# Performance work log

Measured on AMD Instinct MI355X. Metric: run time of the kernel, lower is better.

Reference implementation:

```python
import jax, jax.numpy as jnp
import numpy as np

B = 1024          # number of graphs
H = 8             # heads
EPS = 1e-5        # LayerNorm eps (torch default)
MEAN_RES_SCALE = 0.2


def _ln(x, w, b):
    mu = x.mean(-1, keepdims=True)
    var = ((x - mu) ** 2).mean(-1, keepdims=True)
    return (x - mu) / jnp.sqrt(var + EPS) * w + b


def setup_inputs() -> dict:
    key = jax.random.key(0)
    ks = jax.random.split(key, 10)
    N, D = 262144, 256
    s = 1.0 / np.sqrt(D)
    return {
        "h": jax.random.normal(ks[0], (N, D), jnp.float32),
        "batch": jnp.sort(jax.random.randint(ks[1], (N,), 0, B)),
        "cdr_mask": jax.random.bernoulli(ks[2], 0.2, (N,)),
        "iface_mask": jax.random.bernoulli(ks[3], 0.2, (N,)),
        "ln_kv_w": jnp.ones((D,), jnp.float32),
        "ln_kv_b": jnp.zeros((D,), jnp.float32),
        "ln_q_w": jnp.ones((D,), jnp.float32),
        "ln_q_b": jnp.zeros((D,), jnp.float32),
        "Wk": jax.random.normal(ks[4], (D, D), jnp.float32) * s,
        "Wv": jax.random.normal(ks[5], (D, D), jnp.float32) * s,
        "Wq": jax.random.normal(ks[6], (D, 2 * D), jnp.float32) * (1.0 / np.sqrt(2 * D)),
        "Wres": jax.random.normal(ks[7], (D, D), jnp.float32) * s,
        "Wout": jax.random.normal(ks[8], (D, D), jnp.float32) * s,
        "cdr_bias": jnp.asarray(0.6, jnp.float32),
        "iface_bias": jnp.asarray(0.8, jnp.float32),
        "logit_scale": jnp.asarray(1.0, jnp.float32),
    }


def reference(h, batch, cdr_mask, iface_mask, ln_kv_w, ln_kv_b, ln_q_w, ln_q_b,
              Wk, Wv, Wq, Wres, Wout, cdr_bias, iface_bias, logit_scale):
    N, D = h.shape
    hd = D // H
    # per-graph mean / max pooling (segment reductions; all segments non-empty)
    counts = jax.ops.segment_sum(jnp.ones((N,), h.dtype), batch, num_segments=B)[:, None]
    mean_raw = jax.ops.segment_sum(h, batch, num_segments=B) / counts      # [B,D]
    max_raw = jax.ops.segment_max(h, batch, num_segments=B)                # [B,D]
    # single query per graph (dropout = identity in eval)
    q = jnp.concatenate([mean_raw, max_raw], axis=-1) @ Wq.T               # [B,D]
    q = _ln(q, ln_q_w, ln_q_b).reshape(B, H, hd)                           # [B,H,hd]
    # keys / values per node
    h_ln = _ln(h, ln_kv_w, ln_kv_b)
    k = (h_ln @ Wk.T).reshape(N, H, hd)
    v = (h_ln @ Wv.T).reshape(N, H, hd)
    # attention logits with mask biases
    logit = (k * q[batch]).sum(-1) * (logit_scale / np.sqrt(hd))           # [N,H]
    logit = logit + cdr_bias * cdr_mask.astype(h.dtype)[:, None]
    logit = logit + iface_bias * iface_mask.astype(h.dtype)[:, None]
    # segment softmax over nodes of each graph
    m = jax.ops.segment_max(logit, batch, num_segments=B)                  # [B,H]
    e = jnp.exp(logit - m[batch])
    z = jax.ops.segment_sum(e, batch, num_segments=B)                      # [B,H]
    attn = e / z[batch]                                                    # [N,H]
    g = jax.ops.segment_sum(attn[..., None] * v, batch, num_segments=B)    # [B,H,hd]
    g = g.reshape(B, D)
    return g @ Wout.T + MEAN_RES_SCALE * (mean_raw @ Wres.T)               # [B,D]
```

## Files before the change

### kernel.cpp

```cpp
#include <hip/hip_runtime.h>
#include <math.h>

#define D 256
#define BGRAPH 1024
#define H 8
#define NW 4
#define CDIM 2304

static constexpr float EPS = 1e-5f;
static constexpr float MEAN_RES_SCALE = 0.2f;
static constexpr float INV_SQRT_HD = 0.17677669529663687f;
static constexpr float DEFER_THR = 8.0f;

__global__ void k_offsets(const int* __restrict__ batch, int* __restrict__ offs, int N) {
    int n = blockIdx.x * blockDim.x + threadIdx.x;
    if (n >= N) return;
    int bn = batch[n];
    if (bn < 0) bn = 0;
    if (bn >= BGRAPH) bn = BGRAPH - 1;
    if (n == 0) {
        offs[BGRAPH] = N;
        for (int bb = 0; bb <= bn; ++bb) offs[bb] = 0;
    } else {
        int bp = batch[n - 1];
        if (bp < 0) bp = 0;
        if (bp >= BGRAPH) bp = BGRAPH - 1;
        if (bp != bn)
            for (int bb = bp + 1; bb <= bn; ++bb) offs[bb] = n;
    }
    if (n == N - 1)
        for (int bb = bn + 1; bb < BGRAPH; ++bb) offs[bb] = N;
}

__global__ __launch_bounds__(256) void k_pool(
    const float4* __restrict__ h4, const int* __restrict__ offs,
    const float* __restrict__ Wq, const float* __restrict__ lnq_w,
    const float* __restrict__ lnq_b, const float* __restrict__ Wk,
    const float* __restrict__ logit_scale,
    float* __restrict__ Wkq_g, float* __restrict__ App) {
    __shared__ alignas(16) float psum[NW][D];
    __shared__ alignas(16) float pmax[NW][D];
    __shared__ alignas(16) float cat_s[2 * D];
    __shared__ alignas(16) float q_s[D];
    __shared__ float red_s[2 * NW];

    int b = blockIdx.x;
    int t = threadIdx.x;
    int l = t & 63, w = t >> 6;
    int s = offs[b], e = offs[b + 1];
    int cnt = e - s;

    float4 sum4 = {0.f, 0.f, 0.f, 0.f};
    float4 max4 = {-INFINITY, -INFINITY, -INFINITY, -INFINITY};
    int n = s + w;
    for (; n + NW < e; n += 2 * NW) {
        float4 x0 = h4[(size_t)n * 64 + l];
        float4 x1 = h4[(size_t)(n + NW) * 64 + l];
        sum4.x += x0.x + x1.x; sum4.y += x0.y + x1.y;
        sum4.z += x0.z + x1.z; sum4.w += x0.w + x1.w;
        max4.x = fmaxf(max4.x, fmaxf(x0.x, x1.x));
        max4.y = fmaxf(max4.y, fmaxf(x0.y, x1.y));
        max4.z = fmaxf(max4.z, fmaxf(x0.z, x1.z));
        max4.w = fmaxf(max4.w, fmaxf(x0.w, x1.w));
    }
    if (n < e) {
        float4 x0 = h4[(size_t)n * 64 + l];
        sum4.x += x0.x; sum4.y += x0.y; sum4.z += x0.z; sum4.w += x0.w;
        max4.x = fmaxf(max4.x, x0.x); max4.y = fmaxf(max4.y, x0.y);
        max4.z = fmaxf(max4.z, x0.z); max4.w = fmaxf(max4.w, x0.w);
    }
    *(float4*)&psum[w][4 * l] = sum4;
    *(float4*)&pmax[w][4 * l] = max4;
    __syncthreads();

    int d = t;
    float ssum = psum[0][d] + psum[1][d] + psum[2][d] + psum[3][d];
    float smax = fmaxf(fmaxf(pmax[0][d], pmax[1][d]), fmaxf(pmax[2][d], pmax[3][d]));
    float mean = ssum / (cnt > 0 ? (float)cnt : 1.f);
    if (cnt == 0) { mean = 0.f; smax = 0.f; }
    cat_s[d] = mean;
    cat_s[D + d] = smax;
    App[(size_t)b * CDIM + 2048 + d] = MEAN_RES_SCALE * mean;
    __syncthreads();

    float qp = 0.f;
    const float4* wq4 = (const float4*)(Wq + (size_t)d * 2 * D);
    #pragma unroll 4
    for (int jj = 0; jj < 128; ++jj) {
        float4 wv = wq4[jj];
        float4 cv = *(const float4*)&cat_s[4 * jj];
        qp += wv.x * cv.x + wv.y * cv.y + wv.z * cv.z + wv.w * cv.w;
    }
    float v1 = qp, v2 = qp * qp;
    #pragma unroll
    for (int dd = 1; dd < 64; dd <<= 1) {
        v1 += __shfl_xor(v1, dd);
        v2 += __shfl_xor(v2, dd);
    }
    if (l == 0) { red_s[w] = v1; red_s[NW + w] = v2; }
    __syncthreads();
    float S1 = red_s[0] + red_s[1] + red_s[2] + red_s[3];
    float S2 = red_s[4] + red_s[5] + red_s[6] + red_s[7];
    float mu = S1 * (1.f / D);
    float var = S2 * (1.f / D) - mu * mu;
    float rstd = rsqrtf(var + EPS);
    q_s[d] = (qp - mu) * rstd * lnq_w[d] + lnq_b[d];
    __syncthreads();

    float scale = logit_scale[0] * INV_SQRT_HD;
    int j = t;
    #pragma unroll
    for (int hh = 0; hh < H; ++hh) {
        float acc = 0.f;
        #pragma unroll 8
        for (int r = 0; r < 32; ++r)
            acc += q_s[hh * 32 + r] * Wk[(size_t)(hh * 32 + r) * D + j];
        Wkq_g[(size_t)b * 2048 + hh * D + j] = acc * scale;
    }
}

__device__ __forceinline__ float reduce8(float v[8], int l) {
    {
        bool hi = (l & 1) != 0;
        #pragma unroll
        for (int c = 0; c < 4; ++c) {
            float send = hi ? v[2 * c] : v[2 * c + 1];
            float keep = hi ? v[2 * c + 1] : v[2 * c];
            v[c] = keep + __shfl_xor(send, 1);
        }
    }
    {
        bool hi = (l & 2) != 0;
        #pragma unroll
        for (int c = 0; c < 2; ++c) {
            float send = hi ? v[2 * c] : v[2 * c + 1];
            float keep = hi ? v[2 * c + 1] : v[2 * c];
            v[c] = keep + __shfl_xor(send, 2);
        }
    }
    {
        bool hi = (l & 4) != 0;
        float send = hi ? v[0] : v[1];
        float keep = hi ? v[1] : v[0];
        v[0] = keep + __shfl_xor(send, 4);
    }
    v[0] += __shfl_xor(v[0], 8);
    v[0] += __shfl_xor(v[0], 16);
    v[0] += __shfl_xor(v[0], 32);
    return v[0];
}

__device__ __forceinline__ float reduce2(float a, float b, int l) {
    bool hi = (l & 1) != 0;
    float send = hi ? a : b;
    float keep = hi ? b : a;
    float r = keep + __shfl_xor(send, 1);
    r += __shfl_xor(r, 2);
    r += __shfl_xor(r, 4);
    r += __shfl_xor(r, 8);
    r += __shfl_xor(r, 16);
    r += __shfl_xor(r, 32);
    return r;
}

__global__ __launch_bounds__(256, 4) void k_attn(
    const float4* __restrict__ h4, const int* __restrict__ offs,
    const float* __restrict__ lnkv_w, const float* __restrict__ lnkv_b,
    const int* __restrict__ cdr_mask, const int* __restrict__ iface_mask,
    const float* __restrict__ cdr_bias, const float* __restrict__ iface_bias,
    const float* __restrict__ Wkq_g, float* __restrict__ App) {
    __shared__ union alignas(16) {
        float wkq[H * D];
        float amrg[NW - 1][H * D];
    } u;
    __shared__ alignas(16) float evb[NW][8];
    __shared__ alignas(16) float scb[NW][8];
    __shared__ float mz_s[NW][H];
    __shared__ float zz_s[NW][H];

    int b = blockIdx.x;
    int t = threadIdx.x;
    int l = t & 63, w = t >> 6;
    for (int i = t; i < H * D; i += 256) u.wkq[i] = Wkq_g[(size_t)b * 2048 + i];
    int s = offs[b], e = offs[b + 1];
    float cb = cdr_bias[0], ib = iface_bias[0];
    float4 w4 = *(const float4*)&lnkv_w[4 * l];
    float4 b4 = *(const float4*)&lnkv_b[4 * l];
    __syncthreads();

    if (s == e) {
        for (int i = t; i < H * D; i += 256) App[(size_t)b * CDIM + i] = 0.f;
        return;
    }

    float4 wwkq[H];
    float c1p[H], c0p[H];
    #pragma unroll
    for (int hh = 0; hh < H; ++hh) {
        float4 kq = *(const float4*)&u.wkq[hh * D + 4 * l];
        wwkq[hh].x = w4.x * kq.x; wwkq[hh].y = w4.y * kq.y;
        wwkq[hh].z = w4.z * kq.z; wwkq[hh].w = w4.w * kq.w;
        c1p[hh] = wwkq[hh].x + wwkq[hh].y + wwkq[hh].z + wwkq[hh].w;
        c0p[hh] = b4.x * kq.x + b4.y * kq.y + b4.z * kq.z + b4.w * kq.w;
    }
    float myc1 = reduce8(c1p, l);
    float myc0 = reduce8(c0p, l);

    float mref = -INFINITY, z = 0.f;
    float4 A4[H];
    #pragma unroll
    for (int hh = 0; hh < H; ++hh) A4[hh] = {0.f, 0.f, 0.f, 0.f};

    int n = s + w;
    float4 x = {0.f, 0.f, 0.f, 0.f};
    float bias = 0.f;
    if (n < e) {
        x = h4[(size_t)n * 64 + l];
        bias = cb * (float)cdr_mask[n] + ib * (float)iface_mask[n];
    }
    for (; n < e; n += NW) {
        int n2 = n + NW;
        float4 xn = {0.f, 0.f, 0.f, 0.f};
        float biasn = 0.f;
        if (n2 < e) {
            xn = h4[(size_t)n2 * 64 + l];
            biasn = cb * (float)cdr_mask[n2] + ib * (float)iface_mask[n2];
        }

        float v[8];
        #pragma unroll
        for (int hh = 0; hh < H; ++hh)
            v[hh] = x.x * wwkq[hh].x + x.y * wwkq[hh].y +
                    x.z * wwkq[hh].z + x.w * wwkq[hh].w;
        float s1p = x.x + x.y + x.z + x.w;
        float s2p = x.x * x.x + x.y * x.y + x.z * x.z + x.w * x.w;
        float r = reduce8(v, l);
        float rs = reduce2(s1p, s2p, l);
        float s1 = __shfl(rs, l & ~1);
        float s2 = __shfl(rs, l | 1);
        float mu = s1 * (1.f / D);
        float var = s2 * (1.f / D) - mu * mu;
        float a = rsqrtf(var + EPS);
        float lg = fmaf(r - mu * myc1, a, myc0) + bias;

        unsigned long long need = __ballot(lg > mref + DEFER_THR);
        if (need) {
            float nm = fmaxf(mref, lg);
            float sc = __expf(mref - nm);
            if (l < 8) scb[w][l] = sc;
            mref = nm;
            z *= sc;
            float4 sa = *(float4*)&scb[w][0];
            float4 sb = *(float4*)&scb[w][4];
            A4[0].x *= sa.x; A4[0].y *= sa.x; A4[0].z *= sa.x; A4[0].w *= sa.x;
            A4[1].x *= sa.y; A4[1].y *= sa.y; A4[1].z *= sa.y; A4[1].w *= sa.y;
            A4[2].x *= sa.z; A4[2].y *= sa.z; A4[2].z *= sa.z; A4[2].w *= sa.z;
            A4[3].x *= sa.w; A4[3].y *= sa.w; A4[3].z *= sa.w; A4[3].w *= sa.w;
            A4[4].x *= sb.x; A4[4].y *= sb.x; A4[4].z *= sb.x; A4[4].w *= sb.x;
            A4[5].x *= sb.y; A4[5].y *= sb.y; A4[5].z *= sb.y; A4[5].w *= sb.y;
            A4[6].x *= sb.z; A4[6].y *= sb.z; A4[6].z *= sb.z; A4[6].w *= sb.z;
            A4[7].x *= sb.w; A4[7].y *= sb.w; A4[7].z *= sb.w; A4[7].w *= sb.w;
        }
        float ev = __expf(lg - mref);
        if (l < 8) evb[w][l] = ev;
        z += ev;
        float4 ea = *(float4*)&evb[w][0];
        float4 eb = *(float4*)&evb[w][4];
        float cc = -mu * a;
        float4 hl;
        hl.x = fmaf(fmaf(x.x, a, cc), w4.x, b4.x);
        hl.y = fmaf(fmaf(x.y, a, cc), w4.y, b4.y);
        hl.z = fmaf(fmaf(x.z, a, cc), w4.z, b4.z);
        hl.w = fmaf(fmaf(x.w, a, cc), w4.w, b4.w);
        A4[0].x = fmaf(ea.x, hl.x, A4[0].x); A4[0].y = fmaf(ea.x, hl.y, A4[0].y);
        A4[0].z = fmaf(ea.x, hl.z, A4[0].z); A4[0].w = fmaf(ea.x, hl.w, A4[0].w);
        A4[1].x = fmaf(ea.y, hl.x, A4[1].x); A4[1].y = fmaf(ea.y, hl.y, A4[1].y);
        A4[1].z = fmaf(ea.y, hl.z, A4[1].z); A4[1].w = fmaf(ea.y, hl.w, A4[1].w);
        A4[2].x = fmaf(ea.z, hl.x, A4[2].x); A4[2].y = fmaf(ea.z, hl.y, A4[2].y);
        A4[2].z = fmaf(ea.z, hl.z, A4[2].z); A4[2].w = fmaf(ea.z, hl.w, A4[2].w);
        A4[3].x = fmaf(ea.w, hl.x, A4[3].x); A4[3].y = fmaf(ea.w, hl.y, A4[3].y);
        A4[3].z = fmaf(ea.w, hl.z, A4[3].z); A4[3].w = fmaf(ea.w, hl.w, A4[3].w);
        A4[4].x = fmaf(eb.x, hl.x, A4[4].x); A4[4].y = fmaf(eb.x, hl.y, A4[4].y);
        A4[4].z = fmaf(eb.x, hl.z, A4[4].z); A4[4].w = fmaf(eb.x, hl.w, A4[4].w);
        A4[5].x = fmaf(eb.y, hl.x, A4[5].x); A4[5].y = fmaf(eb.y, hl.y, A4[5].y);
        A4[5].z = fmaf(eb.y, hl.z, A4[5].z); A4[5].w = fmaf(eb.y, hl.w, A4[5].w);
        A4[6].x = fmaf(eb.z, hl.x, A4[6].x); A4[6].y = fmaf(eb.z, hl.y, A4[6].y);
        A4[6].z = fmaf(eb.z, hl.z, A4[6].z); A4[6].w = fmaf(eb.z, hl.w, A4[6].w);
        A4[7].x = fmaf(eb.w, hl.x, A4[7].x); A4[7].y = fmaf(eb.w, hl.y, A4[7].y);
        A4[7].z = fmaf(eb.w, hl.z, A4[7].z); A4[7].w = fmaf(eb.w, hl.w, A4[7].w);

        x = xn; bias = biasn;
    }

    if (l < 8) { mz_s[w][l] = mref; zz_s[w][l] = z; }
    __syncthreads();
    float fw[H], zst[H];
    #pragma unroll
    for (int hh = 0; hh < H; ++hh) {
        float ms = fmaxf(fmaxf(mz_s[0][hh], mz_s[1][hh]), fmaxf(mz_s[2][hh], mz_s[3][hh]));
        float zs = 0.f;
        #pragma unroll
        for (int ww = 0; ww < NW; ++ww) zs += zz_s[ww][hh] * __expf(mz_s[ww][hh] - ms);
        zst[hh] = zs;
        fw[hh] = __expf(mz_s[w][hh] - ms);
    }
    if (w > 0) {
        #pragma unroll
        for (int hh = 0; hh < H; ++hh) {
            float4 r;
            r.x = A4[hh].x * fw[hh]; r.y = A4[hh].y * fw[hh];
            r.z = A4[hh].z * fw[hh]; r.w = A4[hh].w * fw[hh];
            *(float4*)&u.amrg[w - 1][hh * D + 4 * l] = r;
        }
    }
    __syncthreads();
    if (w == 0) {
        #pragma unroll
        for (int hh = 0; hh < H; ++hh) {
            float inv = 1.f / zst[hh];
            int o = hh * D + 4 * l;
            float4 r;
            r.x = (A4[hh].x * fw[hh] + u.amrg[0][o + 0] + u.amrg[1][o + 0] + u.amrg[2][o + 0]) * inv;
            r.y = (A4[hh].y * fw[hh] + u.amrg[0][o + 1] + u.amrg[1][o + 1] + u.amrg[2][o + 1]) * inv;
            r.z = (A4[hh].z * fw[hh] + u.amrg[0][o + 2] + u.amrg[1][o + 2] + u.amrg[2][o + 2]) * inv;
            r.w = (A4[hh].w * fw[hh] + u.amrg[0][o + 3] + u.amrg[1][o + 3] + u.amrg[2][o + 3]) * inv;
            *(float4*)&App[(size_t)b * CDIM + o] = r;
        }
    }
}

__global__ __launch_bounds__(256) void k_T(const float* __restrict__ App,
                                           float* __restrict__ AT) {
    __shared__ float tile[64][65];
    int cb = blockIdx.x;
    int bb = blockIdx.y;
    int t = threadIdx.x;
    int tx = t & 63, ty = t >> 6;
    #pragma unroll
    for (int i = 0; i < 64; i += 4)
        tile[ty + i][tx] = App[(size_t)(bb * 64 + ty + i) * CDIM + cb * 64 + tx];
    __syncthreads();
    #pragma unroll
    for (int i = 0; i < 64; i += 4)
        AT[(size_t)(cb * 64 + ty + i) * BGRAPH + bb * 64 + tx] = tile[tx][ty + i];
}

__global__ __launch_bounds__(256) void k_M(const float* __restrict__ Wv,
                                           const float* __restrict__ Wout,
                                           const float* __restrict__ Wres,
                                           float* __restrict__ M) {
    int c = blockIdx.x;
    int d = threadIdx.x;
    if (c < 2048) {
        int hh = c >> 8, j = c & 255;
        float acc = 0.f;
        #pragma unroll
        for (int r = 0; r < 32; ++r)
            acc += Wv[(size_t)(hh * 32 + r) * D + j] * Wout[(size_t)d * D + hh * 32 + r];
        M[(size_t)c * D + d] = acc;
    } else {
        int j = c - 2048;
        M[(size_t)c * D + d] = Wres[(size_t)d * D + j];
    }
}

__global__ __launch_bounds__(256) void k_out(const float* __restrict__ AT,
                                             const float* __restrict__ Mm,
                                             float* __restrict__ part) {
    int id = blockIdx.x;
    int dchunk = id & 3;
    int btile = (id >> 2) & 15;
    int slice = id >> 6;
    int t = threadIdx.x;
    int lane = t & 63, w = t >> 6;
    int d = dchunk * 64 + lane;
    int b0 = __builtin_amdgcn_readfirstlane(btile * 64 + w * 16);
    int c0 = slice * 288;
    float acc[16];
    #pragma unroll
    for (int i = 0; i < 16; ++i) acc[i] = 0.f;
    for (int c = c0; c < c0 + 288; ++c) {
        float mv = Mm[(size_t)c * D + d];
        const float* ar = AT + (size_t)c * BGRAPH + b0;
        #pragma unroll
        for (int i = 0; i < 16; ++i) acc[i] = fmaf(ar[i], mv, acc[i]);
    }
    #pragma unroll
    for (int i = 0; i < 16; ++i)
        part[((size_t)slice * BGRAPH + b0 + i) * D + d] = acc[i];
}

__global__ __launch_bounds__(256) void k_red(const float* __restrict__ part,
                                             float* __restrict__ out) {
    int i = blockIdx.x * blockDim.x + threadIdx.x;
    const float4* p4 = (const float4*)part;
    float4 a = p4[i];
    #pragma unroll
    for (int s = 1; s < 8; ++s) {
        float4 v = p4[(size_t)s * 65536 + i];
        a.x += v.x; a.y += v.y; a.z += v.z; a.w += v.w;
    }
    ((float4*)out)[i] = a;
}

extern "C" void kernel_launch(void* const* d_in, const int* in_sizes, int n_in,
                              void* d_out, int out_size, void* d_ws, size_t ws_size,
                              hipStream_t stream) {
    const float* h = (const float*)d_in[0];
    const int* batch = (const int*)d_in[1];
    const int* cdr = (const int*)d_in[2];
    const int* ifc = (const int*)d_in[3];
    const float* lnkv_w = (const float*)d_in[4];
    const float* lnkv_b = (const float*)d_in[5];
    const float* lnq_w = (const float*)d_in[6];
    const float* lnq_b = (const float*)d_in[7];
    const float* Wk = (const float*)d_in[8];
    const float* Wv = (const float*)d_in[9];
    const float* Wq = (const float*)d_in[10];
    const float* Wres = (const float*)d_in[11];
    const float* Wout = (const float*)d_in[12];
    const float* cdr_bias = (const float*)d_in[13];
    const float* iface_bias = (const float*)d_in[14];
    const float* logit_scale = (const float*)d_in[15];
    int N = in_sizes[0] / D;

    char* ws = (char*)d_ws;
    size_t o = 0;
    int* offs = (int*)(ws + o);            o += 8192;
    float* Wkq_g = (float*)(ws + o);       o += (size_t)BGRAPH * 2048 * 4;
    float* App = (float*)(ws + o);         o += (size_t)BGRAPH * CDIM * 4;
    float* AT = (float*)(ws + o);          o += (size_t)CDIM * BGRAPH * 4;
    float* Mm = (float*)(ws + o);          o += (size_t)CDIM * D * 4;
    float* part = (float*)(ws + o);        o += (size_t)8 * BGRAPH * D * 4;

    hipLaunchKernelGGL(k_offsets, dim3((N + 255) / 256), dim3(256), 0, stream,
                       batch, offs, N);
    hipLaunchKernelGGL(k_pool, dim3(BGRAPH), dim3(256), 0, stream,
                       (const float4*)h, offs, Wq, lnq_w, lnq_b, Wk, logit_scale,
                       Wkq_g, App);
    hipLaunchKernelGGL(k_attn, dim3(BGRAPH), dim3(256), 0, stream,
                       (const float4*)h, offs, lnkv_w, lnkv_b, cdr, ifc,
                       cdr_bias, iface_bias, Wkq_g, App);
    hipLaunchKernelGGL(k_T, dim3(36, 16), dim3(256), 0, stream, App, AT);
    hipLaunchKernelGGL(k_M, dim3(CDIM), dim3(256), 0, stream, Wv, Wout, Wres, Mm);
    hipLaunchKernelGGL(k_out, dim3(512), dim3(256), 0, stream, AT, Mm, part);
    hipLaunchKernelGGL(k_red, dim3(256), dim3(256), 0, stream, part, (float*)d_out);
}
```

Before: 662.7 us.

## Fuse pooling and query projection into attention kernel, keep Wkq in LDS

Merges the per-graph pooling/query/LN/Wk-projection kernel into the attention kernel so the per-graph key-query vector stays in shared memory instead of round-tripping through global workspace. The second pass over each graph's node rows likely hits L2 because the same block just read them. The pooling loop is unrolled to four rows per iteration, and the weight-combining kernel k_M is launched earlier. The fused kernel uses more shared memory and registers, which may reduce occupancy, and the per-block serial query projection now sits in front of the attention work.

```diff
diff --git a/kernel.cpp b/kernel.cpp
--- a/kernel.cpp
+++ b/kernel.cpp
@@ -32,93 +32,6 @@
         for (int bb = bn + 1; bb < BGRAPH; ++bb) offs[bb] = N;
 }
 
-__global__ __launch_bounds__(256) void k_pool(
-    const float4* __restrict__ h4, const int* __restrict__ offs,
-    const float* __restrict__ Wq, const float* __restrict__ lnq_w,
-    const float* __restrict__ lnq_b, const float* __restrict__ Wk,
-    const float* __restrict__ logit_scale,
-    float* __restrict__ Wkq_g, float* __restrict__ App) {
-    __shared__ alignas(16) float psum[NW][D];
-    __shared__ alignas(16) float pmax[NW][D];
-    __shared__ alignas(16) float cat_s[2 * D];
-    __shared__ alignas(16) float q_s[D];
-    __shared__ float red_s[2 * NW];
-
-    int b = blockIdx.x;
-    int t = threadIdx.x;
-    int l = t & 63, w = t >> 6;
-    int s = offs[b], e = offs[b + 1];
-    int cnt = e - s;
-
-    float4 sum4 = {0.f, 0.f, 0.f, 0.f};
-    float4 max4 = {-INFINITY, -INFINITY, -INFINITY, -INFINITY};
-    int n = s + w;
-    for (; n + NW < e; n += 2 * NW) {
-        float4 x0 = h4[(size_t)n * 64 + l];
-        float4 x1 = h4[(size_t)(n + NW) * 64 + l];
-        sum4.x += x0.x + x1.x; sum4.y += x0.y + x1.y;
-        sum4.z += x0.z + x1.z; sum4.w += x0.w + x1.w;
-        max4.x = fmaxf(max4.x, fmaxf(x0.x, x1.x));
-        max4.y = fmaxf(max4.y, fmaxf(x0.y, x1.y));
-        max4.z = fmaxf(max4.z, fmaxf(x0.z, x1.z));
-        max4.w = fmaxf(max4.w, fmaxf(x0.w, x1.w));
-    }
-    if (n < e) {
-        float4 x0 = h4[(size_t)n * 64 + l];
-        sum4.x += x0.x; sum4.y += x0.y; sum4.z += x0.z; sum4.w += x0.w;
-        max4.x = fmaxf(max4.x, x0.x); max4.y = fmaxf(max4.y, x0.y);
-        max4.z = fmaxf(max4.z, x0.z); max4.w = fmaxf(max4.w, x0.w);
-    }
-    *(float4*)&psum[w][4 * l] = sum4;
-    *(float4*)&pmax[w][4 * l] = max4;
-    __syncthreads();
-
-    int d = t;
-    float ssum = psum[0][d] + psum[1][d] + psum[2][d] + psum[3][d];
-    float smax = fmaxf(fmaxf(pmax[0][d], pmax[1][d]), fmaxf(pmax[2][d], pmax[3][d]));
-    float mean = ssum / (cnt > 0 ? (float)cnt : 1.f);
-    if (cnt == 0) { mean = 0.f; smax = 0.f; }
-    cat_s[d] = mean;
-    cat_s[D + d] = smax;
-    App[(size_t)b * CDIM + 2048 + d] = MEAN_RES_SCALE * mean;
-    __syncthreads();
-
-    float qp = 0.f;
-    const float4* wq4 = (const float4*)(Wq + (size_t)d * 2 * D);
-    #pragma unroll 4
-    for (int jj = 0; jj < 128; ++jj) {
-        float4 wv = wq4[jj];
-        float4 cv = *(const float4*)&cat_s[4 * jj];
-        qp += wv.x * cv.x + wv.y * cv.y + wv.z * cv.z + wv.w * cv.w;
-    }
-    float v1 = qp, v2 = qp * qp;
-    #pragma unroll
-    for (int dd = 1; dd < 64; dd <<= 1) {
-        v1 += __shfl_xor(v1, dd);
-        v2 += __shfl_xor(v2, dd);
-    }
-    if (l == 0) { red_s[w] = v1; red_s[NW + w] = v2; }
-    __syncthreads();
-    float S1 = red_s[0] + red_s[1] + red_s[2] + red_s[3];
-    float S2 = red_s[4] + red_s[5] + red_s[6] + red_s[7];
-    float mu = S1 * (1.f / D);
-    float var = S2 * (1.f / D) - mu * mu;
-    float rstd = rsqrtf(var + EPS);
-    q_s[d] = (qp - mu) * rstd * lnq_w[d] + lnq_b[d];
-    __syncthreads();
-
-    float scale = logit_scale[0] * INV_SQRT_HD;
-    int j = t;
-    #pragma unroll
-    for (int hh = 0; hh < H; ++hh) {
-        float acc = 0.f;
-        #pragma unroll 8
-        for (int r = 0; r < 32; ++r)
-            acc += q_s[hh * 32 + r] * Wk[(size_t)(hh * 32 + r) * D + j];
-        Wkq_g[(size_t)b * 2048 + hh * D + j] = acc * scale;
-    }
-}
-
 __device__ __forceinline__ float reduce8(float v[8], int l) {
     {
         bool hi = (l & 1) != 0;
@@ -163,16 +76,23 @@
     return r;
 }
 
-__global__ __launch_bounds__(256, 4) void k_attn(
+__global__ __launch_bounds__(256, 4) void k_fused(
     const float4* __restrict__ h4, const int* __restrict__ offs,
+    const float* __restrict__ Wq, const float* __restrict__ lnq_w,
+    const float* __restrict__ lnq_b, const float* __restrict__ Wk,
+    const float* __restrict__ logit_scale,
     const float* __restrict__ lnkv_w, const float* __restrict__ lnkv_b,
     const int* __restrict__ cdr_mask, const int* __restrict__ iface_mask,
     const float* __restrict__ cdr_bias, const float* __restrict__ iface_bias,
-    const float* __restrict__ Wkq_g, float* __restrict__ App) {
+    float* __restrict__ App) {
     __shared__ union alignas(16) {
+        struct { float psum[NW][D]; float pmax[NW][D]; } p;
         float wkq[H * D];
         float amrg[NW - 1][H * D];
     } u;
+    __shared__ alignas(16) float cat_s[2 * D];
+    __shared__ alignas(16) float q_s[D];
+    __shared__ float red_s[2 * NW];
     __shared__ alignas(16) float evb[NW][8];
     __shared__ alignas(16) float scb[NW][8];
     __shared__ float mz_s[NW][H];
@@ -181,17 +101,100 @@
     int b = blockIdx.x;
     int t = threadIdx.x;
     int l = t & 63, w = t >> 6;
-    for (int i = t; i < H * D; i += 256) u.wkq[i] = Wkq_g[(size_t)b * 2048 + i];
     int s = offs[b], e = offs[b + 1];
-    float cb = cdr_bias[0], ib = iface_bias[0];
+    int cnt = e - s;
     float4 w4 = *(const float4*)&lnkv_w[4 * l];
     float4 b4 = *(const float4*)&lnkv_b[4 * l];
+    float cb = cdr_bias[0], ib = iface_bias[0];
+
+    float4 sum4 = {0.f, 0.f, 0.f, 0.f};
+    float4 max4 = {-INFINITY, -INFINITY, -INFINITY, -INFINITY};
+    {
+        int n = s + w;
+        for (; n + 3 * NW < e; n += 4 * NW) {
+            float4 x0 = h4[(size_t)n * 64 + l];
+            float4 x1 = h4[(size_t)(n + NW) * 64 + l];
+            float4 x2 = h4[(size_t)(n + 2 * NW) * 64 + l];
+            float4 x3 = h4[(size_t)(n + 3 * NW) * 64 + l];
+            sum4.x += (x0.x + x1.x) + (x2.x + x3.x);
+            sum4.y += (x0.y + x1.y) + (x2.y + x3.y);
+            sum4.z += (x0.z + x1.z) + (x2.z + x3.z);
+            sum4.w += (x0.w + x1.w) + (x2.w + x3.w);
+            max4.x = fmaxf(max4.x, fmaxf(fmaxf(x0.x, x1.x), fmaxf(x2.x, x3.x)));
+            max4.y = fmaxf(max4.y, fmaxf(fmaxf(x0.y, x1.y), fmaxf(x2.y, x3.y)));
+            max4.z = fmaxf(max4.z, fmaxf(fmaxf(x0.z, x1.z), fmaxf(x2.z, x3.z)));
+            max4.w = fmaxf(max4.w, fmaxf(fmaxf(x0.w, x1.w), fmaxf(x2.w, x3.w)));
+        }
+        for (; n < e; n += NW) {
+            float4 x0 = h4[(size_t)n * 64 + l];
+            sum4.x += x0.x; sum4.y += x0.y; sum4.z += x0.z; sum4.w += x0.w;
+            max4.x = fmaxf(max4.x, x0.x); max4.y = fmaxf(max4.y, x0.y);
+            max4.z = fmaxf(max4.z, x0.z); max4.w = fmaxf(max4.w, x0.w);
+        }
+    }
+    *(float4*)&u.p.psum[w][4 * l] = sum4;
+    *(float4*)&u.p.pmax[w][4 * l] = max4;
+    __syncthreads();
+
+    {
+        int d = t;
+        float ssum = u.p.psum[0][d] + u.p.psum[1][d] + u.p.psum[2][d] + u.p.psum[3][d];
+        float smax = fmaxf(fmaxf(u.p.pmax[0][d], u.p.pmax[1][d]),
+                           fmaxf(u.p.pmax[2][d], u.p.pmax[3][d]));
+        float mean = ssum / (cnt > 0 ? (float)cnt : 1.f);
+        if (cnt == 0) { mean = 0.f; smax = 0.f; }
+        cat_s[d] = mean;
+        cat_s[D + d] = smax;
+        App[(size_t)b * CDIM + 2048 + d] = MEAN_RES_SCALE * mean;
+    }
     __syncthreads();
 
     if (s == e) {
         for (int i = t; i < H * D; i += 256) App[(size_t)b * CDIM + i] = 0.f;
         return;
     }
+
+    float qp = 0.f;
+    {
+        const float4* wq4 = (const float4*)(Wq + (size_t)t * 2 * D);
+        #pragma unroll 4
+        for (int jj = 0; jj < 128; ++jj) {
+            float4 wv = wq4[jj];
+            float4 cv = *(const float4*)&cat_s[4 * jj];
+            qp += wv.x * cv.x + wv.y * cv.y + wv.z * cv.z + wv.w * cv.w;
+        }
+    }
+    float v1 = qp, v2 = qp * qp;
+    #pragma unroll
+    for (int dd = 1; dd < 64; dd <<= 1) {
+        v1 += __shfl_xor(v1, dd);
+        v2 += __shfl_xor(v2, dd);
+    }
+    if (l == 0) { red_s[w] = v1; red_s[NW + w] = v2; }
+    __syncthreads();
+    {
+        float S1 = red_s[0] + red_s[1] + red_s[2] + red_s[3];
+        float S2 = red_s[4] + red_s[5] + red_s[6] + red_s[7];
+        float mu = S1 * (1.f / D);
+        float var = S2 * (1.f / D) - mu * mu;
+        float rstd = rsqrtf(var + EPS);
+        q_s[t] = (qp - mu) * rstd * lnq_w[t] + lnq_b[t];
+    }
+    __syncthreads();
+
+    {
+        float scale = logit_scale[0] * INV_SQRT_HD;
+        int j = t;
+        #pragma unroll
+        for (int hh = 0; hh < H; ++hh) {
+            float acc = 0.f;
+            #pragma unroll 8
+            for (int r = 0; r < 32; ++r)
+                acc += q_s[hh * 32 + r] * Wk[(size_t)(hh * 32 + r) * D + j];
+            u.wkq[hh * D + j] = acc * scale;
+        }
+    }
+    __syncthreads();
 
     float4 wwkq[H];
     float c1p[H], c0p[H];
@@ -427,7 +430,6 @@
     char* ws = (char*)d_ws;
     size_t o = 0;
     int* offs = (int*)(ws + o);            o += 8192;
-    float* Wkq_g = (float*)(ws + o);       o += (size_t)BGRAPH * 2048 * 4;
     float* App = (float*)(ws + o);         o += (size_t)BGRAPH * CDIM * 4;
     float* AT = (float*)(ws + o);          o += (size_t)CDIM * BGRAPH * 4;
     float* Mm = (float*)(ws + o);          o += (size_t)CDIM * D * 4;
@@ -435,14 +437,11 @@
 
     hipLaunchKernelGGL(k_offsets, dim3((N + 255) / 256), dim3(256), 0, stream,
                        batch, offs, N);
-    hipLaunchKernelGGL(k_pool, dim3(BGRAPH), dim3(256), 0, stream,
+    hipLaunchKernelGGL(k_M, dim3(CDIM), dim3(256), 0, stream, Wv, Wout, Wres, Mm);
+    hipLaunchKernelGGL(k_fused, dim3(BGRAPH), dim3(256), 0, stream,
                        (const float4*)h, offs, Wq, lnq_w, lnq_b, Wk, logit_scale,
-                       Wkq_g, App);
-    hipLaunchKernelGGL(k_attn, dim3(BGRAPH), dim3(256), 0, stream,
-                       (const float4*)h, offs, lnkv_w, lnkv_b, cdr, ifc,
-                       cdr_bias, iface_bias, Wkq_g, App);
+                       lnkv_w, lnkv_b, cdr, ifc, cdr_bias, iface_bias, App);
     hipLaunchKernelGGL(k_T, dim3(36, 16), dim3(256), 0, stream, App, AT);
-    hipLaunchKernelGGL(k_M, dim3(CDIM), dim3(256), 0, stream, Wv, Wout, Wres, Mm);
     hipLaunchKernelGGL(k_out, dim3(512), dim3(256), 0, stream, AT, Mm, part);
     hipLaunchKernelGGL(k_red, dim3(256), dim3(256), 0, stream, part, (float*)d_out);
 }
```

Result: slower. 679.8 us (+2.6%).
